# Performance work log

Hardware: AMD Instinct MI355X
Metric: run time of the kernel (lower is better)

Reference implementation:

```python
import jax, jax.numpy as jnp
import numpy as np

VOCAB = 1000
PAD_ID = 0
D = 256      # d_model
H = 256      # hidden_size
G = 4 * H    # LSTM gate width
B = 64
S = 256      # src_len
TGT = 257    # tgt_len (decode T = 256)


def setup_inputs() -> dict:
    key = jax.random.key(0)
    ks = iter(jax.random.split(key, 48))
    def p(shape, scale):
        return jax.random.normal(next(ks), shape, jnp.float32) * scale
    inp = {}
    inp['src'] = jax.random.randint(next(ks), (B, S), 1, VOCAB)    # no PAD tokens
    inp['tgt'] = jax.random.randint(next(ks), (B, TGT), 1, VOCAB)
    inp['emb'] = p((VOCAB, D), D ** -0.5).at[PAD_ID].set(0.0)       # padding_idx row zeroed
    s = 1.0 / np.sqrt(H)
    # encoder biLSTM: layer0 fwd/bwd (input D), layer1 fwd/bwd (input 2H)
    for name, din in [('e0f', D), ('e0b', D), ('e1f', 2 * H), ('e1b', 2 * H)]:
        inp[name + '_Wih'] = p((G, din), 1.0 / np.sqrt(din))
        inp[name + '_Whh'] = p((G, H), s)
        inp[name + '_bih'] = p((G,), s)
        inp[name + '_bhh'] = p((G,), s)
    # decoder LSTM: layer0 input D+2H, layer1 input H
    for name, din in [('d0', D + 2 * H), ('d1', H)]:
        inp[name + '_Wih'] = p((G, din), 1.0 / np.sqrt(din))
        inp[name + '_Whh'] = p((G, H), s)
        inp[name + '_bih'] = p((G,), s)
        inp[name + '_bhh'] = p((G,), s)
    inp['h_proj_W'] = p((H, 2 * H), 1.0 / np.sqrt(2 * H))
    inp['h_proj_b'] = p((H,), s)
    inp['c_proj_W'] = p((H, 2 * H), 1.0 / np.sqrt(2 * H))
    inp['c_proj_b'] = p((H,), s)
    inp['att_Wenc'] = p((H, 2 * H), 1.0 / np.sqrt(2 * H))
    inp['att_Wdec'] = p((H, H), s)
    inp['att_v'] = p((H,), s)
    return inp


def _cell(gates, c):
    # PyTorch gate order: i, f, g, o
    i, f, g, o = jnp.split(gates, 4, axis=-1)
    c = jax.nn.sigmoid(f) * c + jax.nn.sigmoid(i) * jnp.tanh(g)
    return jax.nn.sigmoid(o) * jnp.tanh(c), c


def _lstm(x, Wih, Whh, bih, bhh, reverse=False):
    # x: (B, S, din) -> outputs (B, S, H), final (h, c)
    Bsz = x.shape[0]
    Hd = Whh.shape[1]
    pre = jnp.swapaxes(x @ Wih.T + bih + bhh, 0, 1)  # (S, B, 4H)
    def step(carry, g):
        h, c = carry
        h, c = _cell(g + h @ Whh.T, c)
        return (h, c), h
    init = (jnp.zeros((Bsz, Hd), x.dtype), jnp.zeros((Bsz, Hd), x.dtype))
    (hT, cT), ys = jax.lax.scan(step, init, pre, reverse=reverse)
    return jnp.swapaxes(ys, 0, 1), hT, cT


def reference(src, tgt, emb,
              e0f_Wih, e0f_Whh, e0f_bih, e0f_bhh,
              e0b_Wih, e0b_Whh, e0b_bih, e0b_bhh,
              e1f_Wih, e1f_Whh, e1f_bih, e1f_bhh,
              e1b_Wih, e1b_Whh, e1b_bih, e1b_bhh,
              d0_Wih, d0_Whh, d0_bih, d0_bhh,
              d1_Wih, d1_Whh, d1_bih, d1_bhh,
              h_proj_W, h_proj_b, c_proj_W, c_proj_b,
              att_Wenc, att_Wdec, att_v):
    mask = (src == PAD_ID)                       # (B, S), all False here
    x0 = emb[src]                                # (B, S, D)
    # ---- bidirectional 2-layer encoder ----
    f0, _, _ = _lstm(x0, e0f_Wih, e0f_Whh, e0f_bih, e0f_bhh)
    b0, _, _ = _lstm(x0, e0b_Wih, e0b_Whh, e0b_bih, e0b_bhh, reverse=True)
    x1 = jnp.concatenate([f0, b0], axis=-1)      # (B, S, 2H)
    f1, hf, cf = _lstm(x1, e1f_Wih, e1f_Whh, e1f_bih, e1f_bhh)
    b1, hb, cb = _lstm(x1, e1b_Wih, e1b_Whh, e1b_bih, e1b_bhh, reverse=True)
    enc_out = jnp.concatenate([f1, b1], axis=-1)  # (B, S, 2H)
    # ---- decoder init (shared across both decoder layers) ----
    h0 = jnp.tanh(jnp.concatenate([hf, hb], -1) @ h_proj_W.T + h_proj_b)
    c0 = jnp.tanh(jnp.concatenate([cf, cb], -1) @ c_proj_W.T + c_proj_b)
    # ---- teacher-forced decode with Bahdanau attention ----
    enc_proj = enc_out @ att_Wenc.T              # (B, S, H), hoisted out of the loop
    tgt_emb = emb[tgt[:, :-1]]                   # (B, T, D)

    def dec_step(carry, xt):
        hl0, cl0, hl1, cl1 = carry
        energy = jnp.tanh(enc_proj + (hl1 @ att_Wdec.T)[:, None, :])  # (B, S, H)
        scores = energy @ att_v                                        # (B, S)
        scores = jnp.where(mask, -jnp.inf, scores)
        w = jax.nn.softmax(scores, axis=-1)
        ctx = jnp.einsum('bs,bse->be', w, enc_out)                     # (B, 2H)
        x = jnp.concatenate([xt, ctx], axis=-1)                        # (B, D+2H)
        hl0, cl0 = _cell(x @ d0_Wih.T + d0_bih + d0_bhh + hl0 @ d0_Whh.T, cl0)
        hl1, cl1 = _cell(hl0 @ d1_Wih.T + d1_bih + d1_bhh + hl1 @ d1_Whh.T, cl1)
        return (hl0, cl0, hl1, cl1), hl1

    _, outs = jax.lax.scan(dec_step, (h0, c0, h0, c0), jnp.swapaxes(tgt_emb, 0, 1))
    out = jnp.swapaxes(outs, 0, 1)               # (B, T, H); out_proj is None (H == D)
    return out @ emb.T                           # weight-tied fc_out -> (B, T, VOCAB)
```

## Files before the change

### kernel.cpp

```cpp
#include <hip/hip_runtime.h>
#include <hip/hip_bf16.h>
#include <stdint.h>

#define B_ 64
#define S_ 256
#define T_ 256
#define D_ 256
#define H_ 256
#define V_ 1000

__device__ __forceinline__ float blo(unsigned u){ return __uint_as_float(u << 16); }
__device__ __forceinline__ float bhi(unsigned u){ return __uint_as_float(u & 0xffff0000u); }
__device__ __forceinline__ float sigm(float x){ return 1.0f / (1.0f + __expf(-x)); }
__device__ __forceinline__ float tanhfast(float x){ float e = __expf(2.0f * x); return 1.0f - 2.0f / (e + 1.0f); }

__device__ __forceinline__ void cellupd(float a0, float a1, float a2, float a3, float& c, float& h){
  float cn = sigm(a1) * c + sigm(a0) * tanhfast(a2);
  c = cn;
  h = sigm(a3) * tanhfast(cn);
}

__device__ __forceinline__ float wredmax(float v){
  #pragma unroll
  for (int o = 32; o > 0; o >>= 1) v = fmaxf(v, __shfl_xor(v, o));
  return v;
}
__device__ __forceinline__ float wredsum(float v){
  #pragma unroll
  for (int o = 32; o > 0; o >>= 1) v += __shfl_xor(v, o);
  return v;
}

__device__ __forceinline__ void ast(float* p, float v){
  __hip_atomic_store(p, v, __ATOMIC_RELAXED, __HIP_MEMORY_SCOPE_AGENT);
}
__device__ __forceinline__ float ald(const float* p){
  return __hip_atomic_load(p, __ATOMIC_RELAXED, __HIP_MEMORY_SCOPE_AGENT);
}

__global__ void probe_kernel(const unsigned short* __restrict__ w, int* __restrict__ flag)
{
  int cnt = 0;
  for (int i = threadIdx.x; i < 4096; i += 64) {
    unsigned e = (w[i] >> 7) & 0xFFu;
    if (e >= 0xC0u) cnt++;
  }
  #pragma unroll
  for (int o = 32; o > 0; o >>= 1) cnt += __shfl_xor(cnt, o);
  if (threadIdx.x == 0) *flag = (cnt > 32) ? 1 : 0;
}

__device__ __forceinline__ float load_any(const void* src, int i, int isf32){
  return isf32 ? ((const float*)src)[i]
               : __uint_as_float(((unsigned)((const unsigned short*)src)[i]) << 16);
}

__global__ void conv_kernel(const void* __restrict__ src, float* __restrict__ dst, int n,
                            const int* __restrict__ flagp)
{
  int i = blockIdx.x * 256 + threadIdx.x;
  if (i >= n) return;
  dst[i] = load_any(src, i, *flagp);
}

__global__ void bias_kernel(const void* __restrict__ a, const void* __restrict__ bsrc,
                            float* __restrict__ dst, int n, const int* __restrict__ flagp)
{
  int i = blockIdx.x * 256 + threadIdx.x;
  if (i >= n) return;
  int f = *flagp;
  dst[i] = load_any(a, i, f) + load_any(bsrc, i, f);
}

__global__ void swzb_kernel(const void* __restrict__ src, unsigned short* __restrict__ dst,
                            int R, int Ks, int Kt, int c0, int perm, const int* __restrict__ flagp)
{
  int i = blockIdx.x * 256 + threadIdx.x;
  if (i >= R * Ks) return;
  int r = i / Ks;
  int k = i - r * Ks;
  int kk = k + c0;
  int Rr = r;
  if (perm) {
    int g = r >> 8, j = r & 255;
    Rr = ((j >> 4) << 6) + (g << 4) + (j & 15);
  }
  float v = load_any(src, i, *flagp);
  __hip_bfloat16 bv = __float2bfloat16(v);
  dst[(((size_t)(Rr >> 6) * (size_t)(Kt >> 3) + (size_t)(kk >> 3)) * 64 + (Rr & 63)) * 8 + (kk & 7)] =
      *(unsigned short*)&bv;
}

template<int K>
__device__ __forceinline__ float dot1w(const unsigned short* __restrict__ w, int r,
                                       const float* __restrict__ xs)
{
  constexpr int KC = K >> 3;
  const uint4* __restrict__ p = (const uint4*)w + (size_t)(r >> 6) * KC * 64 + (r & 63);
  float a = 0.0f;
  #pragma unroll 4
  for (int kc = 0; kc < KC; ++kc) {
    const uint4 q = p[(size_t)kc * 64];
    const float4 x0 = *(const float4*)(xs + kc * 8);
    const float4 x1 = *(const float4*)(xs + kc * 8 + 4);
    a += blo(q.x)*x0.x + bhi(q.x)*x0.y + blo(q.y)*x0.z + bhi(q.y)*x0.w
       + blo(q.z)*x1.x + bhi(q.z)*x1.y + blo(q.w)*x1.z + bhi(q.w)*x1.w;
  }
  return a;
}

template<int KC, int SL>
__device__ __forceinline__ void dot4s(const unsigned short* __restrict__ w, int j, int q,
                                      const float* __restrict__ xsl, float out4[4])
{
  const int lane = j & 63, wq = j >> 6;
  const uint4* __restrict__ p0 = (const uint4*)w + ((size_t)(wq     ) * KC + q * SL) * 64 + lane;
  const uint4* __restrict__ p1 = (const uint4*)w + ((size_t)(wq + 4 ) * KC + q * SL) * 64 + lane;
  const uint4* __restrict__ p2 = (const uint4*)w + ((size_t)(wq + 8 ) * KC + q * SL) * 64 + lane;
  const uint4* __restrict__ p3 = (const uint4*)w + ((size_t)(wq + 12) * KC + q * SL) * 64 + lane;
  float a0 = 0.0f, a1 = 0.0f, a2 = 0.0f, a3 = 0.0f;
  #pragma unroll 4
  for (int kc = 0; kc < SL; ++kc) {
    const float4 x0 = *(const float4*)(xsl + kc * 8);
    const float4 x1 = *(const float4*)(xsl + kc * 8 + 4);
    uint4 qq;
    qq = p0[(size_t)kc * 64];
    a0 += blo(qq.x)*x0.x + bhi(qq.x)*x0.y + blo(qq.y)*x0.z + bhi(qq.y)*x0.w
        + blo(qq.z)*x1.x + bhi(qq.z)*x1.y + blo(qq.w)*x1.z + bhi(qq.w)*x1.w;
    qq = p1[(size_t)kc * 64];
    a1 += blo(qq.x)*x0.x + bhi(qq.x)*x0.y + blo(qq.y)*x0.z + bhi(qq.y)*x0.w
        + blo(qq.z)*x1.x + bhi(qq.z)*x1.y + blo(qq.w)*x1.z + bhi(qq.w)*x1.w;
    qq = p2[(size_t)kc * 64];
    a2 += blo(qq.x)*x0.x + bhi(qq.x)*x0.y + blo(qq.y)*x0.z + bhi(qq.y)*x0.w
        + blo(qq.z)*x1.x + bhi(qq.z)*x1.y + blo(qq.w)*x1.z + bhi(qq.w)*x1.w;
    qq = p3[(size_t)kc * 64];
    a3 += blo(qq.x)*x0.x + bhi(qq.x)*x0.y + blo(qq.y)*x0.z + bhi(qq.y)*x0.w
        + blo(qq.z)*x1.x + bhi(qq.z)*x1.y + blo(qq.w)*x1.z + bhi(qq.w)*x1.w;
  }
  out4[0] = a0; out4[1] = a1; out4[2] = a2; out4[3] = a3;
}

__global__ __launch_bounds__(1024, 1) void enc0_kernel(
    const int* __restrict__ src, const float* __restrict__ emb_f,
    const unsigned short* __restrict__ wF, const unsigned short* __restrict__ wB,
    const float* __restrict__ bF, const float* __restrict__ bB,
    float* __restrict__ f0, float* __restrict__ b0)
{
  const int blk = blockIdx.x, dir = blk >> 6, b = blk & 63, tid = threadIdx.x;
  const unsigned short* w = dir ? wB : wF;
  const float* bi = dir ? bB : bF;
  float* outp = dir ? b0 : f0;
  __shared__ __align__(16) float xs[512];
  __shared__ __align__(16) float work4[4096];
  const int q = tid >> 8, j = tid & 255;
  float bias_g[4];
  if (tid < 256) {
    #pragma unroll
    for (int g = 0; g < 4; ++g) bias_g[g] = bi[g * 256 + tid];
    xs[256 + tid] = 0.0f;
  }
  float c = 0.0f, h = 0.0f;
  const size_t bS = (size_t)b * S_;
  for (int t = 0; t < S_; ++t) {
    const int tp = dir ? (S_ - 1 - t) : t;
    const int tok = src[bS + tp];
    if (tid < 256) xs[tid] = emb_f[(size_t)tok * D_ + tid];
    __syncthreads();
    float o4[4];
    dot4s<64, 16>(w, j, q, xs + q * 128, o4);
    #pragma unroll
    for (int g = 0; g < 4; ++g) work4[(g * 4 + q) * 256 + j] = o4[g];
    __syncthreads();
    if (tid < 256) {
      float gv[4];
      #pragma unroll
      for (int g = 0; g < 4; ++g)
        gv[g] = work4[(g*4+0)*256 + tid] + work4[(g*4+1)*256 + tid]
              + work4[(g*4+2)*256 + tid] + work4[(g*4+3)*256 + tid] + bias_g[g];
      cellupd(gv[0], gv[1], gv[2], gv[3], c, h);
      xs[256 + tid] = h;
      outp[(bS + tp) * H_ + tid] = h;
    }
    __syncthreads();
  }
}

__global__ __launch_bounds__(1024, 1) void enc1_kernel(
    const float* __restrict__ f0, const float* __restrict__ b0,
    const unsigned short* __restrict__ wF, const unsigned short* __restrict__ wB,
    const float* __restrict__ bF, const float* __restrict__ bB,
    float* __restrict__ enc_out, float* __restrict__ hcbuf)
{
  const int blk = blockIdx.x, dir = blk >> 6, b = blk & 63, tid = threadIdx.x;
  const unsigned short* w = dir ? wB : wF;
  const float* bi = dir ? bB : bF;
  __shared__ __align__(16) float xs[768];
  __shared__ __align__(16) float work4[4096];
  const int q = tid >> 8, j = tid & 255;
  float bias_g[4];
  if (tid < 256) {
    #pragma unroll
    for (int g = 0; g < 4; ++g) bias_g[g] = bi[g * 256 + tid];
    xs[512 + tid] = 0.0f;
  }
  float c = 0.0f, h = 0.0f;
  const size_t bS = (size_t)b * S_;
  for (int t = 0; t < S_; ++t) {
    const int tp = dir ? (S_ - 1 - t) : t;
    const size_t row = (bS + tp) * (size_t)H_;
    if (tid < 512) {
      const int jj = tid & 255;
      xs[tid] = (tid < 256) ? f0[row + jj] : b0[row + jj];
    }
    __syncthreads();
    float o4[4];
    dot4s<96, 24>(w, j, q, xs + q * 192, o4);
    #pragma unroll
    for (int g = 0; g < 4; ++g) work4[(g * 4 + q) * 256 + j] = o4[g];
    __syncthreads();
    if (tid < 256) {
      float gv[4];
      #pragma unroll
      for (int g = 0; g < 4; ++g)
        gv[g] = work4[(g*4+0)*256 + tid] + work4[(g*4+1)*256 + tid]
              + work4[(g*4+2)*256 + tid] + work4[(g*4+3)*256 + tid] + bias_g[g];
      cellupd(gv[0], gv[1], gv[2], gv[3], c, h);
      xs[512 + tid] = h;
      enc_out[(bS + tp) * 512 + dir * 256 + tid] = h;
    }
    __syncthreads();
  }
  if (tid < 256) {
    const int BH = B_ * H_;
    float* hout = hcbuf + (dir ? 2 * BH : 0);
    hout[(size_t)b * H_ + tid]      = h;
    hout[BH + (size_t)b * H_ + tid] = c;
  }
}

__global__ __launch_bounds__(256) void proj_kernel(
    const float* __restrict__ enc_out, const float* __restrict__ hcbuf,
    const unsigned short* __restrict__ wenc_s,
    const unsigned short* __restrict__ hpw_s, const unsigned short* __restrict__ cpw_s,
    const float* __restrict__ hpb_f, const float* __restrict__ cpb_f,
    float* __restrict__ epT, float* __restrict__ h0c0)
{
  __shared__ __align__(16) float xs[16 * 512];
  const int blk = blockIdx.x, tid = threadIdx.x;
  if (blk < 1024) {
    const int b = blk >> 4, s0 = (blk & 15) * 16;
    const float* srcp = enc_out + ((size_t)b * S_ + s0) * 512;
    for (int i = tid; i < 16 * 512; i += 256) xs[i] = srcp[i];
    __syncthreads();
    float acc[16];
    #pragma unroll
    for (int r = 0; r < 16; ++r) acc[r] = 0.0f;
    const uint4* p = (const uint4*)wenc_s + (size_t)(tid >> 6) * 64 * 64 + (tid & 63);
    for (int kc = 0; kc < 64; ++kc) {
      const uint4 q = p[(size_t)kc * 64];
      const float w0=blo(q.x), w1=bhi(q.x), w2=blo(q.y), w3=bhi(q.y),
                  w4=blo(q.z), w5=bhi(q.z), w6=blo(q.w), w7=bhi(q.w);
      #pragma unroll
      for (int r = 0; r < 16; ++r) {
        const float4 x0 = *(const float4*)(xs + r * 512 + kc * 8);
        const float4 x1 = *(const float4*)(xs + r * 512 + kc * 8 + 4);
        acc[r] += w0*x0.x + w1*x0.y + w2*x0.z + w3*x0.w + w4*x1.x + w5*x1.y + w6*x1.z + w7*x1.w;
      }
    }
    float* dst = epT + ((size_t)b * S_ + (size_t)tid) * 256 + s0;
    #pragma unroll
    for (int r = 0; r < 16; ++r) dst[r] = acc[r];
  } else {
    const int b = blk - 1024;
    const int BH = B_ * H_;
    xs[tid]        = hcbuf[(size_t)b * H_ + tid];
    xs[256 + tid]  = hcbuf[2 * BH + (size_t)b * H_ + tid];
    xs[512 + tid]  = hcbuf[BH + (size_t)b * H_ + tid];
    xs[768 + tid]  = hcbuf[3 * BH + (size_t)b * H_ + tid];
    __syncthreads();
    const float hv = dot1w<512>(hpw_s, tid, xs)       + hpb_f[tid];
    const float cv = dot1w<512>(cpw_s, tid, xs + 512) + cpb_f[tid];
    h0c0[(size_t)b * H_ + tid]              = tanhfast(hv);
    h0c0[(size_t)BH + (size_t)b * H_ + tid] = tanhfast(cv);
  }
}

__global__ __launch_bounds__(256) void gemb_kernel(
    const float* __restrict__ emb_f, const unsigned short* __restrict__ d0p,
    float* __restrict__ gemb)
{
  __shared__ __align__(16) float xs[16 * 256];
  const int blk = blockIdx.x, tg = blk >> 2, cg = blk & 3, tid = threadIdx.x;
  for (int i = tid; i < 16 * 256; i += 256) {
    const int tk = tg * 16 + (i >> 8);
    xs[i] = (tk < V_) ? emb_f[(size_t)tk * 256 + (i & 255)] : 0.0f;
  }
  __syncthreads();
  const int r = cg * 256 + tid;
  const uint4* p = (const uint4*)d0p + (size_t)(r >> 6) * 128 * 64 + (r & 63);
  float acc[16];
  #pragma unroll
  for (int ti = 0; ti < 16; ++ti) acc[ti] = 0.0f;
  for (int kc = 0; kc < 32; ++kc) {
    const uint4 q = p[(size_t)kc * 64];
    const float w0=blo(q.x), w1=bhi(q.x), w2=blo(q.y), w3=bhi(q.y),
                w4=blo(q.z), w5=bhi(q.z), w6=blo(q.w), w7=bhi(q.w);
    #pragma unroll
    for (int ti = 0; ti < 16; ++ti) {
      const float4 x0 = *(const float4*)(xs + ti * 256 + kc * 8);
      const float4 x1 = *(const float4*)(xs + ti * 256 + kc * 8 + 4);
      acc[ti] += w0*x0.x + w1*x0.y + w2*x0.z + w3*x0.w + w4*x1.x + w5*x1.y + w6*x1.z + w7*x1.w;
    }
  }
  #pragma unroll
  for (int ti = 0; ti < 16; ++ti) {
    const int tk = tg * 16 + ti;
    if (tk < V_) gemb[(size_t)tk * 1024 + r] = acc[ti];
  }
}

__global__ void zero_cnt_kernel(int* __restrict__ cnt)
{
  for (int i = threadIdx.x; i < 2048; i += 256) cnt[i] = 0;
}

__global__ __launch_bounds__(1024, 1) void dec_fused_kernel(
    const int* __restrict__ src, const int* __restrict__ tgt,
    const float* __restrict__ h0c0,
    const float* __restrict__ epT, const float* __restrict__ enc_out,
    const float* __restrict__ gemb,
    const unsigned short* __restrict__ wdec_s,
    const unsigned short* __restrict__ d0p, const unsigned short* __restrict__ d1p,
    const float* __restrict__ d0b, const float* __restrict__ d1b,
    const float* __restrict__ attv_f,
    float* __restrict__ dec_h,
    float* __restrict__ esc, float* __restrict__ ctxg,
    float* __restrict__ hl0g, float* __restrict__ hl1g,
    int* __restrict__ cnt)
{
  const int Bk = blockIdx.x, b = Bk >> 2, k = Bk & 3, tid = threadIdx.x;
  const int j64 = k * 64;

  __shared__ __align__(16) float epl[256 * 65];
  __shared__ __align__(16) unsigned short eol[128 * 264];
  __shared__ __align__(16) float work[1024];
  __shared__ __align__(16) float workF[1024];
  __shared__ __align__(16) float xs0[768];
  __shared__ __align__(16) float hl1s[256];
  __shared__ __align__(16) float hl0n[256];
  __shared__ __align__(16) float qloc[64];
  __shared__ __align__(16) float vv[64];
  __shared__ __align__(16) float msk[256];
  __shared__ __align__(16) float wsm[256];
  __shared__ __align__(16) float cl0s[64];
  __shared__ __align__(16) float cl1s[64];
  __shared__ float red[16];

  const float* epb = epT + (size_t)b * (S_ * 256);
  const float* eob = enc_out + (size_t)b * (S_ * 512);

  for (int i = tid; i < 256 * 64; i += 1024) {
    const int s = i & 255, jj = i >> 8;
    epl[s * 65 + jj] = epb[(size_t)(j64 + jj) * 256 + s];
  }
  for (int i = tid; i < 128 * 256; i += 1024) {
    const int dl = i & 127, s = i >> 7;
    __hip_bfloat16 bv = __float2bfloat16(eob[(size_t)s * 512 + k * 128 + dl]);
    eol[dl * 264 + s] = *(unsigned short*)&bv;
  }
  if (tid < 256) {
    msk[tid] = (src[b * 256 + tid] == 0) ? -1e30f : 0.0f;
    const float h0 = h0c0[b * 256 + tid];
    hl1s[tid] = h0;
    xs0[512 + tid] = h0;
  }
  float b0r[4], b1r[4];
  if (tid < 64) {
    vv[tid] = attv_f[j64 + tid];
    const float c0 = h0c0[B_ * H_ + b * 256 + j64 + tid];
    cl0s[tid] = c0; cl1s[tid] = c0;
    #pragma unroll
    for (int g = 0; g < 4; ++g) {
      b0r[g] = d0b[g * 256 + j64 + tid];
      b1r[g] = d1b[g * 256 + j64 + tid];
    }
  }
  __syncthreads();

  int syncno = 0;
#define ARRIVE() do {                                                                    \
    ++syncno;                                                                            \
    __syncthreads();     \
    if (tid == 0)                                                                        \
      __hip_atomic_fetch_add(&cnt[b * 32], 1, __ATOMIC_RELAXED, __HIP_MEMORY_SCOPE_AGENT); \
  } while (0)
#define WAIT() do {                                                                      \
    if (tid == 0) {                                                                      \
      while (__hip_atomic_load(&cnt[b * 32], __ATOMIC_RELAXED, __HIP_MEMORY_SCOPE_AGENT) \
             < 4 * syncno)                                                               \
        __builtin_amdgcn_s_sleep(1);                                                     \
    }                                                                                    \
    __syncthreads();                                                                     \
    asm volatile("" ::: "memory");                                                       \
  } while (0)

  const int lr = tid & 255, q4 = tid >> 8;
  const int gg4 = lr >> 6, jj4 = lr & 63;
  const uint4* __restrict__ d0pb = (const uint4*)d0p + (size_t)(gg4 * 4 + k) * 128 * 64 + jj4;
  const uint4* __restrict__ d1pb = (const uint4*)d1p + (size_t)(gg4 * 4 + k) * 64 * 64 + jj4;

  for (int t = 0; t < T_; ++t) {
    float gpre[4];
    if (tid < 64) {
      const float* ge = gemb + (size_t)tgt[b * 257 + t] * 1024;
      #pragma unroll
      for (int g = 0; g < 4; ++g)
        gpre[g] = __builtin_nontemporal_load(ge + g * 256 + j64 + tid);
    }

    {
      const int jj = tid & 63, q16 = tid >> 6;
      const uint4* p = (const uint4*)wdec_s + ((size_t)k * 32 + q16 * 2) * 64 + jj;
      const float* xsl = hl1s + q16 * 16;
      const uint4 w0 = p[0], w1 = p[64];
      const float4 xa = *(const float4*)(xsl);
      const float4 xb = *(const float4*)(xsl + 4);
      const float4 xc = *(const float4*)(xsl + 8);
      const float4 xd = *(const float4*)(xsl + 12);
      const float a =
          blo(w0.x)*xa.x + bhi(w0.x)*xa.y + blo(w0.y)*xa.z + bhi(w0.y)*xa.w
        + blo(w0.z)*xb.x + bhi(w0.z)*xb.y + blo(w0.w)*xb.z + bhi(w0.w)*xb.w
        + blo(w1.x)*xc.x + bhi(w1.x)*xc.y + blo(w1.y)*xc.z + bhi(w1.y)*xc.w
        + blo(w1.z)*xd.x + bhi(w1.z)*xd.y + blo(w1.w)*xd.z + bhi(w1.w)*xd.w;
      work[q16 * 64 + jj] = a;
    }
    __syncthreads();
    if (tid < 64) {
      float q = 0.0f;
      #pragma unroll
      for (int i = 0; i < 16; ++i) q += work[i * 64 + tid];
      qloc[tid] = q;
    }
    __syncthreads();

    {
      const int s = tid & 255, jq = tid >> 8;
      const float* ep = epl + s * 65 + jq * 16;
      const float* qv = qloc + jq * 16;
      const float* vp = vv + jq * 16;
      float a = 0.0f;
      #pragma unroll
      for (int i = 0; i < 16; ++i)
        a += vp[i] * tanhfast(ep[i] + qv[i]);
      work[jq * 256 + s] = a;
    }
    __syncthreads();
    if (tid < 256)
      ast(&esc[b * 1024 + k * 256 + tid],
          work[tid] + work[256 + tid] + work[512 + tid] + work[768 + tid]);
    ARRIVE();

    {
      const uint4* p = d0pb + (size_t)(96 + q4 * 8) * 64;
      const float* xsl = xs0 + 512 + q4 * 64;
      float a = 0.0f;
      #pragma unroll
      for (int kc = 0; kc < 8; ++kc) {
        const uint4 w = p[(size_t)kc * 64];
        const float4 x0 = *(const float4*)(xsl + kc * 8);
        const float4 x1 = *(const float4*)(xsl + kc * 8 + 4);
        a += blo(w.x)*x0.x + bhi(w.x)*x0.y + blo(w.y)*x0.z + bhi(w.y)*x0.w
           + blo(w.z)*x1.x + bhi(w.z)*x1.y + blo(w.w)*x1.z + bhi(w.w)*x1.w;
      }
      work[q4 * 256 + lr] = a;
    }
    WAIT();

    {
      float e = -1e30f;
      if (tid < 256) {
        const float* eb = esc + b * 1024;
        e = ald(&eb[tid]) + ald(&eb[256 + tid]) + ald(&eb[512 + tid]) + ald(&eb[768 + tid])
          + msk[tid];
      }
      const float m0 = wredmax(e);
      if (tid < 256 && (tid & 63) == 0) red[tid >> 6] = m0;
      __syncthreads();
      const float m = fmaxf(fmaxf(red[0], red[1]), fmaxf(red[2], red[3]));
      const float pe = (tid < 256) ? __expf(e - m) : 0.0f;
      const float ss = wredsum(pe);
      if (tid < 256 && (tid & 63) == 0) red[4 + (tid >> 6)] = ss;
      __syncthreads();
      const float inv = 1.0f / ((red[4] + red[5]) + (red[6] + red[7]));
      if (tid < 256) wsm[tid] = pe * inv;
    }
    __syncthreads();

    {
      const int dq = tid & 127, sg = tid >> 7;
      const uint4* er = (const uint4*)(eol + dq * 264 + sg * 32);
      const float* wp = wsm + sg * 32;
      float a = 0.0f;
      #pragma unroll
      for (int i4 = 0; i4 < 4; ++i4) {
        const uint4 q = er[i4];
        const float* w8 = wp + i4 * 8;
        a += blo(q.x)*w8[0] + bhi(q.x)*w8[1] + blo(q.y)*w8[2] + bhi(q.y)*w8[3]
           + blo(q.z)*w8[4] + bhi(q.z)*w8[5] + blo(q.w)*w8[6] + bhi(q.w)*w8[7];
      }
      workF[sg * 128 + dq] = a;
    }
    __syncthreads();
    if (tid < 128) {
      float a = 0.0f;
      #pragma unroll
      for (int g = 0; g < 8; ++g) a += workF[g * 128 + tid];
      ast(&ctxg[b * 512 + k * 128 + tid], a);
    }
    ARRIVE();

    {
      const uint4* p = d1pb + (size_t)(32 + q4 * 8) * 64;
      const float* xsl = hl1s + q4 * 64;
      float a = 0.0f;
      #pragma unroll
      for (int kc = 0; kc < 8; ++kc) {
        const uint4 w = p[(size_t)kc * 64];
        const float4 x0 = *(const float4*)(xsl + kc * 8);
        const float4 x1 = *(const float4*)(xsl + kc * 8 + 4);
        a += blo(w.x)*x0.x + bhi(w.x)*x0.y + blo(w.y)*x0.z + bhi(w.y)*x0.w
           + blo(w.z)*x1.x + bhi(w.z)*x1.y + blo(w.w)*x1.z + bhi(w.w)*x1.w;
      }
      workF[q4 * 256 + lr] = a;
    }
    WAIT();
    if (tid < 512) xs0[tid] = ald(&ctxg[b * 512 + tid]);
    __syncthreads();

    {
      const uint4* p = d0pb + (size_t)(32 + q4 * 16) * 64;
      const float* xsl = xs0 + q4 * 128;
      float a = 0.0f;
      #pragma unroll 8
      for (int kc = 0; kc < 16; ++kc) {
        const uint4 w = p[(size_t)kc * 64];
        const float4 x0 = *(const float4*)(xsl + kc * 8);
        const float4 x1 = *(const float4*)(xsl + kc * 8 + 4);
        a += blo(w.x)*x0.x + bhi(w.x)*x0.y + blo(w.y)*x0.z + bhi(w.y)*x0.w
           + blo(w.z)*x1.x + bhi(w.z)*x1.y + blo(w.w)*x1.z + bhi(w.w)*x1.w;
      }
      work[q4 * 256 + lr] += a;
    }
    __syncthreads();
    if (tid < 64) {
      float gv[4];
      #pragma unroll
      for (int g = 0; g < 4; ++g) {
        const int r = g * 64 + tid;
        gv[g] = work[r] + work[256 + r] + work[512 + r] + work[768 + r]
              + b0r[g] + gpre[g];
      }
      float c = cl0s[tid], h;
      cellupd(gv[0], gv[1], gv[2], gv[3], c, h);
      cl0s[tid] = c;
      ast(&hl0g[b * 256 + j64 + tid], h);
    }
    ARRIVE();
    WAIT();
    if (tid < 256) {
      const float hv = ald(&hl0g[b * 256 + tid]);
      hl0n[tid] = hv;
      xs0[512 + tid] = hv;
    }
    __syncthreads();

    {
      const uint4* p = d1pb + (size_t)(q4 * 8) * 64;
      const float* xsl = hl0n + q4 * 64;
      float a = 0.0f;
      #pragma unroll
      for (int kc = 0; kc < 8; ++kc) {
        const uint4 w = p[(size_t)kc * 64];
        const float4 x0 = *(const float4*)(xsl + kc * 8);
        const float4 x1 = *(const float4*)(xsl + kc * 8 + 4);
        a += blo(w.x)*x0.x + bhi(w.x)*x0.y + blo(w.y)*x0.z + bhi(w.y)*x0.w
           + blo(w.z)*x1.x + bhi(w.z)*x1.y + blo(w.w)*x1.z + bhi(w.w)*x1.w;
      }
      workF[q4 * 256 + lr] += a;
    }
    __syncthreads();
    if (tid < 64) {
      float gv[4];
      #pragma unroll
      for (int g = 0; g < 4; ++g) {
        const int r = g * 64 + tid;
        gv[g] = workF[r] + workF[256 + r] + workF[512 + r] + workF[768 + r] + b1r[g];
      }
      float c = cl1s[tid], h;
      cellupd(gv[0], gv[1], gv[2], gv[3], c, h);
      cl1s[tid] = c;
      ast(&hl1g[b * 256 + j64 + tid], h);
      __builtin_nontemporal_store(h, &dec_h[((size_t)b * T_ + t) * H_ + j64 + tid]);
    }
    ARRIVE();
    WAIT();
    if (tid < 256) hl1s[tid] = ald(&hl1g[b * 256 + tid]);
    __syncthreads();
  }
#undef ARRIVE
#undef WAIT
}

__global__ __launch_bounds__(256) void out_kernel(
    const float* __restrict__ dec_h, const unsigned short* __restrict__ emb_s,
    void* __restrict__ out, const int* __restrict__ flagp)
{
  __shared__ __align__(16) float hs[16 * 256];
  const int blk = blockIdx.x, tid = threadIdx.x;
  const int isf32 = *flagp;
  const float* srcp = dec_h + (size_t)blk * (16 * 256);
  for (int i = tid; i < 16 * 256; i += 256) hs[i] = srcp[i];
  __syncthreads();
  #pragma unroll
  for (int vi = 0; vi < 4; ++vi) {
    const int v = tid + vi * 256;
    if (v < V_) {
      const uint4* p = (const uint4*)emb_s + (size_t)(v >> 6) * 32 * 64 + (v & 63);
      float acc[16];
      #pragma unroll
      for (int r = 0; r < 16; ++r) acc[r] = 0.0f;
      for (int kc = 0; kc < 32; ++kc) {
        const uint4 q = p[(size_t)kc * 64];
        const float w0=blo(q.x), w1=bhi(q.x), w2=blo(q.y), w3=bhi(q.y),
                    w4=blo(q.z), w5=bhi(q.z), w6=blo(q.w), w7=bhi(q.w);
        #pragma unroll
        for (int r = 0; r < 16; ++r) {
          const float4 x0 = *(const float4*)(hs + r * 256 + kc * 8);
          const float4 x1 = *(const float4*)(hs + r * 256 + kc * 8 + 4);
          acc[r] += w0*x0.x + w1*x0.y + w2*x0.z + w3*x0.w + w4*x1.x + w5*x1.y + w6*x1.z + w7*x1.w;
        }
      }
      const size_t rowbase = (size_t)blk * 16;
      if (isf32) {
        float* o = (float*)out;
        #pragma unroll
        for (int r = 0; r < 16; ++r) o[(rowbase + r) * V_ + v] = acc[r];
      } else {
        __hip_bfloat16* o = (__hip_bfloat16*)out;
        #pragma unroll
        for (int r = 0; r < 16; ++r) o[(rowbase + r) * V_ + v] = __float2bfloat16(acc[r]);
      }
    }
  }
}

extern "C" void kernel_launch(void* const* d_in, const int* in_sizes, int n_in,
                              void* d_out, int out_size, void* d_ws, size_t ws_size,
                              hipStream_t stream)
{
  (void)in_sizes; (void)n_in; (void)out_size; (void)ws_size;
  const int* src = (const int*)d_in[0];
  const int* tgt = (const int*)d_in[1];

  char* base = (char*)d_ws;
  int* flag = (int*)base;
  float* ws = (float*)(base + 256);
  size_t off = 0;
  float* f0      = ws + off; off += (size_t)B_ * S_ * H_;
  float* b0      = ws + off; off += (size_t)B_ * S_ * H_;
  float* enc_out = ws + off; off += (size_t)B_ * S_ * 2 * H_;
  float* hcbuf   = ws + off; off += 4 * (size_t)B_ * H_;
  float* h0c0    = ws + off; off += 2 * (size_t)B_ * H_;
  float* emb_f   = ws + off; off += (size_t)V_ * D_;
  float* gemb    = ws + off; off += (size_t)V_ * 1024;
  float* esc     = ws + off; off += (size_t)B_ * S_ * 4;
  float* ctxg    = ws + off; off += (size_t)B_ * 512;
  float* hl0g    = ws + off; off += (size_t)B_ * H_;
  float* hl1g    = ws + off; off += (size_t)B_ * H_;
  int*   cntp    = (int*)(ws + off); off += 2048;
  float* e0f_b   = ws + off; off += 1024;
  float* e0b_b   = ws + off; off += 1024;
  float* e1f_b   = ws + off; off += 1024;
  float* e1b_b   = ws + off; off += 1024;
  float* d0_b    = ws + off; off += 1024;
  float* d1_b    = ws + off; off += 1024;
  float* hpb_f   = ws + off; off += 256;
  float* cpb_f   = ws + off; off += 256;
  float* attv_f  = ws + off; off += 256;
  unsigned short* us = (unsigned short*)(ws + off);
  size_t uo = 0;
  unsigned short* e0f_s  = us + uo; uo += (size_t)1024 * 512;
  unsigned short* e0b_s  = us + uo; uo += (size_t)1024 * 512;
  unsigned short* e1f_s  = us + uo; uo += (size_t)1024 * 768;
  unsigned short* e1b_s  = us + uo; uo += (size_t)1024 * 768;
  unsigned short* d0p_s  = us + uo; uo += (size_t)1024 * 1024;
  unsigned short* d1p_s  = us + uo; uo += (size_t)1024 * 512;
  unsigned short* wdec_s = us + uo; uo += (size_t)256 * 256;
  unsigned short* wenc_s = us + uo; uo += (size_t)256 * 512;
  unsigned short* hpw_s  = us + uo; uo += (size_t)256 * 512;
  unsigned short* cpw_s  = us + uo; uo += (size_t)256 * 512;
  unsigned short* emb_s  = us + uo; uo += (size_t)1024 * 256;
  float* dec_h = f0;
  float* epT   = b0;

  hipLaunchKernelGGL(probe_kernel, dim3(1), dim3(64), 0, stream,
                     (const unsigned short*)d_in[3], flag);

  auto swz = [&](int idx, unsigned short* dst, int R, int Ks, int Kt, int c0, int perm){
    const int n = R * Ks;
    hipLaunchKernelGGL(swzb_kernel, dim3((n + 255) / 256), dim3(256), 0, stream,
                       d_in[idx], dst, R, Ks, Kt, c0, perm, flag);
  };
  auto bias2 = [&](int ia, int ib, float* dst, int n){
    hipLaunchKernelGGL(bias_kernel, dim3((n + 255) / 256), dim3(256), 0, stream,
                       d_in[ia], d_in[ib], dst, n, flag);
  };

  hipLaunchKernelGGL(conv_kernel, dim3((V_ * D_ + 255) / 256), dim3(256), 0, stream,
                     d_in[2], emb_f, V_ * D_, flag);
  hipLaunchKernelGGL(conv_kernel, dim3(1), dim3(256), 0, stream, d_in[28], hpb_f, 256, flag);
  hipLaunchKernelGGL(conv_kernel, dim3(1), dim3(256), 0, stream, d_in[30], cpb_f, 256, flag);
  hipLaunchKernelGGL(conv_kernel, dim3(1), dim3(256), 0, stream, d_in[33], attv_f, 256, flag);
  bias2(5, 6, e0f_b, 1024);   bias2(9, 10, e0b_b, 1024);
  bias2(13, 14, e1f_b, 1024); bias2(17, 18, e1b_b, 1024);
  bias2(21, 22, d0_b, 1024);  bias2(25, 26, d1_b, 1024);
  swz(3,  e0f_s, 1024, 256, 512, 0, 0);   swz(4,  e0f_s, 1024, 256, 512, 256, 0);
  swz(7,  e0b_s, 1024, 256, 512, 0, 0);   swz(8,  e0b_s, 1024, 256, 512, 256, 0);
  swz(11, e1f_s, 1024, 512, 768, 0, 0);   swz(12, e1f_s, 1024, 256, 768, 512, 0);
  swz(15, e1b_s, 1024, 512, 768, 0, 0);   swz(16, e1b_s, 1024, 256, 768, 512, 0);
  swz(19, d0p_s, 1024, 768, 1024, 0, 0);  swz(20, d0p_s, 1024, 256, 1024, 768, 0);
  swz(23, d1p_s, 1024, 256, 512, 0, 0);   swz(24, d1p_s, 1024, 256, 512, 256, 0);
  swz(32, wdec_s, 256, 256, 256, 0, 0);
  swz(31, wenc_s, 256, 512, 512, 0, 0);
  swz(27, hpw_s, 256, 512, 512, 0, 0);
  swz(29, cpw_s, 256, 512, 512, 0, 0);
  swz(2,  emb_s, 1000, 256, 256, 0, 0);

  hipLaunchKernelGGL(gemb_kernel, dim3(252), dim3(256), 0, stream, emb_f, d0p_s, gemb);

  hipLaunchKernelGGL(enc0_kernel, dim3(128), dim3(1024), 0, stream,
                     src, emb_f, e0f_s, e0b_s, e0f_b, e0b_b, f0, b0);
  hipLaunchKernelGGL(enc1_kernel, dim3(128), dim3(1024), 0, stream,
                     f0, b0, e1f_s, e1b_s, e1f_b, e1b_b, enc_out, hcbuf);
  hipLaunchKernelGGL(proj_kernel, dim3(1088), dim3(256), 0, stream,
                     enc_out, hcbuf, wenc_s, hpw_s, cpw_s, hpb_f, cpb_f, epT, h0c0);

  hipLaunchKernelGGL(zero_cnt_kernel, dim3(1), dim3(256), 0, stream, cntp);

  {
    const int* srcp_ = src; const int* tgtp_ = tgt;
    const float* h0c0_ = h0c0; const float* epT_ = epT; const float* eo_ = enc_out;
    const float* gemb_ = gemb;
    const unsigned short* wdec_ = wdec_s;
    const unsigned short* d0p_ = d0p_s; const unsigned short* d1p_ = d1p_s;
    const float* d0b_ = d0_b; const float* d1b_ = d1_b; const float* attv_ = attv_f;
    float* dech_ = dec_h; float* esc_ = esc; float* ctxg_ = ctxg;
    float* hl0g_ = hl0g; float* hl1g_ = hl1g; int* cnt_ = cntp;
    void* kargs[] = {
      (void*)&srcp_, (void*)&tgtp_, (void*)&h0c0_, (void*)&epT_, (void*)&eo_,
      (void*)&gemb_, (void*)&wdec_, (void*)&d0p_, (void*)&d1p_,
      (void*)&d0b_, (void*)&d1b_, (void*)&attv_,
      (void*)&dech_, (void*)&esc_, (void*)&ctxg_, (void*)&hl0g_, (void*)&hl1g_, (void*)&cnt_
    };
    hipError_t e = hipLaunchCooperativeKernel((const void*)dec_fused_kernel,
                                              dim3(256), dim3(1024), kargs, 0, stream);
    if (e != hipSuccess) {
      hipLaunchKernelGGL(dec_fused_kernel, dim3(256), dim3(1024), 0, stream,
                         srcp_, tgtp_, h0c0_, epT_, eo_, gemb_, wdec_, d0p_, d1p_,
                         d0b_, d1b_, attv_, dech_, esc_, ctxg_, hl0g_, hl1g_, cnt_);
    }
  }

  hipLaunchKernelGGL(out_kernel, dim3(1024), dim3(256), 0, stream,
                     dec_h, emb_s, d_out, flag);
}
```

Baseline: 13.75 ms.

## Split decoder per batch across 8 smaller blocks with XCD-aware mapping

```diff
diff --git a/kernel.cpp b/kernel.cpp
--- a/kernel.cpp
+++ b/kernel.cpp
@@ -324,7 +324,7 @@
   for (int i = threadIdx.x; i < 2048; i += 256) cnt[i] = 0;
 }
 
-__global__ __launch_bounds__(1024, 1) void dec_fused_kernel(
+__global__ __launch_bounds__(512, 4) void dec_fused_kernel(
     const int* __restrict__ src, const int* __restrict__ tgt,
     const float* __restrict__ h0c0,
     const float* __restrict__ epT, const float* __restrict__ enc_out,
@@ -338,34 +338,36 @@
     float* __restrict__ hl0g, float* __restrict__ hl1g,
     int* __restrict__ cnt)
 {
-  const int Bk = blockIdx.x, b = Bk >> 2, k = Bk & 3, tid = threadIdx.x;
-  const int j64 = k * 64;
-
-  __shared__ __align__(16) float epl[256 * 65];
-  __shared__ __align__(16) unsigned short eol[128 * 264];
-  __shared__ __align__(16) float work[1024];
-  __shared__ __align__(16) float workF[1024];
+  const int Bk = blockIdx.x, tid = threadIdx.x;
+  const int xcd = Bk >> 6, i64 = Bk & 63;
+  const int b = xcd * 8 + (i64 & 7), k = i64 >> 3;
+  const int j32 = k * 32, d64 = k * 64;
+
+  __shared__ __align__(16) float epl[256 * 33];
+  __shared__ __align__(16) unsigned short eol[64 * 264];
+  __shared__ __align__(16) float work[512];
+  __shared__ __align__(16) float workF[512];
   __shared__ __align__(16) float xs0[768];
   __shared__ __align__(16) float hl1s[256];
   __shared__ __align__(16) float hl0n[256];
-  __shared__ __align__(16) float qloc[64];
-  __shared__ __align__(16) float vv[64];
+  __shared__ __align__(16) float qloc[32];
+  __shared__ __align__(16) float vv[32];
   __shared__ __align__(16) float msk[256];
   __shared__ __align__(16) float wsm[256];
-  __shared__ __align__(16) float cl0s[64];
-  __shared__ __align__(16) float cl1s[64];
+  __shared__ __align__(16) float cl0s[32];
+  __shared__ __align__(16) float cl1s[32];
   __shared__ float red[16];
 
   const float* epb = epT + (size_t)b * (S_ * 256);
   const float* eob = enc_out + (size_t)b * (S_ * 512);
 
-  for (int i = tid; i < 256 * 64; i += 1024) {
+  for (int i = tid; i < 256 * 32; i += 512) {
     const int s = i & 255, jj = i >> 8;
-    epl[s * 65 + jj] = epb[(size_t)(j64 + jj) * 256 + s];
-  }
-  for (int i = tid; i < 128 * 256; i += 1024) {
-    const int dl = i & 127, s = i >> 7;
-    __hip_bfloat16 bv = __float2bfloat16(eob[(size_t)s * 512 + k * 128 + dl]);
+    epl[s * 33 + jj] = epb[(size_t)(j32 + jj) * 256 + s];
+  }
+  for (int i = tid; i < 64 * 256; i += 512) {
+    const int dl = i & 63, s = i >> 6;
+    __hip_bfloat16 bv = __float2bfloat16(eob[(size_t)s * 512 + d64 + dl]);
     eol[dl * 264 + s] = *(unsigned short*)&bv;
   }
   if (tid < 256) {
@@ -375,14 +377,14 @@
     xs0[512 + tid] = h0;
   }
   float b0r[4], b1r[4];
-  if (tid < 64) {
-    vv[tid] = attv_f[j64 + tid];
-    const float c0 = h0c0[B_ * H_ + b * 256 + j64 + tid];
+  if (tid < 32) {
+    vv[tid] = attv_f[j32 + tid];
+    const float c0 = h0c0[B_ * H_ + b * 256 + j32 + tid];
     cl0s[tid] = c0; cl1s[tid] = c0;
     #pragma unroll
     for (int g = 0; g < 4; ++g) {
-      b0r[g] = d0b[g * 256 + j64 + tid];
-      b1r[g] = d1b[g * 256 + j64 + tid];
+      b0r[g] = d0b[g * 256 + j32 + tid];
+      b1r[g] = d1b[g * 256 + j32 + tid];
     }
   }
   __syncthreads();
@@ -397,32 +399,35 @@
 #define WAIT() do {                                                                      \
     if (tid == 0) {                                                                      \
       while (__hip_atomic_load(&cnt[b * 32], __ATOMIC_RELAXED, __HIP_MEMORY_SCOPE_AGENT) \
-             < 4 * syncno)                                                               \
+             < 8 * syncno)                                                               \
         __builtin_amdgcn_s_sleep(1);                                                     \
     }                                                                                    \
     __syncthreads();                                                                     \
     asm volatile("" ::: "memory");                                                       \
   } while (0)
 
-  const int lr = tid & 255, q4 = tid >> 8;
-  const int gg4 = lr >> 6, jj4 = lr & 63;
-  const uint4* __restrict__ d0pb = (const uint4*)d0p + (size_t)(gg4 * 4 + k) * 128 * 64 + jj4;
-  const uint4* __restrict__ d1pb = (const uint4*)d1p + (size_t)(gg4 * 4 + k) * 64 * 64 + jj4;
+  const int lr = tid & 127, q4 = tid >> 7;
+  const int g4 = lr >> 5, jj32 = lr & 31;
+  const int lane = ((k & 1) << 5) + jj32;
+  const int rg0 = g4 * 4 + (k >> 1);
+  const uint4* __restrict__ d0pb = (const uint4*)d0p + (size_t)rg0 * 128 * 64 + lane;
+  const uint4* __restrict__ d1pb = (const uint4*)d1p + (size_t)rg0 * 64 * 64 + lane;
+  const int jjA = tid & 31, q16 = tid >> 5;
+  const uint4* __restrict__ wAp = (const uint4*)wdec_s
+      + ((size_t)(k >> 1) * 32 + q16 * 2) * 64 + (((k & 1) << 5) + jjA);
 
   for (int t = 0; t < T_; ++t) {
     float gpre[4];
-    if (tid < 64) {
+    if (tid < 32) {
       const float* ge = gemb + (size_t)tgt[b * 257 + t] * 1024;
       #pragma unroll
       for (int g = 0; g < 4; ++g)
-        gpre[g] = __builtin_nontemporal_load(ge + g * 256 + j64 + tid);
+        gpre[g] = __builtin_nontemporal_load(ge + g * 256 + j32 + tid);
     }
 
     {
-      const int jj = tid & 63, q16 = tid >> 6;
-      const uint4* p = (const uint4*)wdec_s + ((size_t)k * 32 + q16 * 2) * 64 + jj;
       const float* xsl = hl1s + q16 * 16;
-      const uint4 w0 = p[0], w1 = p[64];
+      const uint4 w0 = wAp[0], w1 = wAp[64];
       const float4 xa = *(const float4*)(xsl);
       const float4 xb = *(const float4*)(xsl + 4);
       const float4 xc = *(const float4*)(xsl + 8);
@@ -432,20 +437,20 @@
         + blo(w0.z)*xb.x + bhi(w0.z)*xb.y + blo(w0.w)*xb.z + bhi(w0.w)*xb.w
         + blo(w1.x)*xc.x + bhi(w1.x)*xc.y + blo(w1.y)*xc.z + bhi(w1.y)*xc.w
         + blo(w1.z)*xd.x + bhi(w1.z)*xd.y + blo(w1.w)*xd.z + bhi(w1.w)*xd.w;
-      work[q16 * 64 + jj] = a;
-    }
-    __syncthreads();
-    if (tid < 64) {
+      work[q16 * 32 + jjA] = a;
+    }
+    __syncthreads();
+    if (tid < 32) {
       float q = 0.0f;
       #pragma unroll
-      for (int i = 0; i < 16; ++i) q += work[i * 64 + tid];
+      for (int i = 0; i < 16; ++i) q += work[i * 32 + tid];
       qloc[tid] = q;
     }
     __syncthreads();
 
     {
       const int s = tid & 255, jq = tid >> 8;
-      const float* ep = epl + s * 65 + jq * 16;
+      const float* ep = epl + s * 33 + jq * 16;
       const float* qv = qloc + jq * 16;
       const float* vp = vv + jq * 16;
       float a = 0.0f;
@@ -456,8 +461,7 @@
     }
     __syncthreads();
     if (tid < 256)
-      ast(&esc[b * 1024 + k * 256 + tid],
-          work[tid] + work[256 + tid] + work[512 + tid] + work[768 + tid]);
+      ast(&esc[b * 2048 + k * 256 + tid], work[tid] + work[256 + tid]);
     ARRIVE();
 
     {
@@ -472,16 +476,17 @@
         a += blo(w.x)*x0.x + bhi(w.x)*x0.y + blo(w.y)*x0.z + bhi(w.y)*x0.w
            + blo(w.z)*x1.x + bhi(w.z)*x1.y + blo(w.w)*x1.z + bhi(w.w)*x1.w;
       }
-      work[q4 * 256 + lr] = a;
+      work[q4 * 128 + lr] = a;
     }
     WAIT();
 
     {
       float e = -1e30f;
       if (tid < 256) {
-        const float* eb = esc + b * 1024;
-        e = ald(&eb[tid]) + ald(&eb[256 + tid]) + ald(&eb[512 + tid]) + ald(&eb[768 + tid])
-          + msk[tid];
+        const float* eb = esc + b * 2048;
+        e = msk[tid];
+        #pragma unroll
+        for (int kk = 0; kk < 8; ++kk) e += ald(&eb[kk * 256 + tid]);
       }
       const float m0 = wredmax(e);
       if (tid < 256 && (tid & 63) == 0) red[tid >> 6] = m0;
@@ -497,7 +502,7 @@
     __syncthreads();
 
     {
-      const int dq = tid & 127, sg = tid >> 7;
+      const int dq = tid & 63, sg = tid >> 6;
       const uint4* er = (const uint4*)(eol + dq * 264 + sg * 32);
       const float* wp = wsm + sg * 32;
       float a = 0.0f;
@@ -508,14 +513,14 @@
         a += blo(q.x)*w8[0] + bhi(q.x)*w8[1] + blo(q.y)*w8[2] + bhi(q.y)*w8[3]
            + blo(q.z)*w8[4] + bhi(q.z)*w8[5] + blo(q.w)*w8[6] + bhi(q.w)*w8[7];
       }
-      workF[sg * 128 + dq] = a;
-    }
-    __syncthreads();
-    if (tid < 128) {
+      workF[sg * 64 + dq] = a;
+    }
+    __syncthreads();
+    if (tid < 64) {
       float a = 0.0f;
       #pragma unroll
-      for (int g = 0; g < 8; ++g) a += workF[g * 128 + tid];
-      ast(&ctxg[b * 512 + k * 128 + tid], a);
+      for (int g = 0; g < 8; ++g) a += workF[g * 64 + tid];
+      ast(&ctxg[b * 512 + d64 + tid], a);
     }
     ARRIVE();
 
@@ -531,10 +536,10 @@
         a += blo(w.x)*x0.x + bhi(w.x)*x0.y + blo(w.y)*x0.z + bhi(w.y)*x0.w
            + blo(w.z)*x1.x + bhi(w.z)*x1.y + blo(w.w)*x1.z + bhi(w.w)*x1.w;
       }
-      workF[q4 * 256 + lr] = a;
+      workF[q4 * 128 + lr] = a;
     }
     WAIT();
-    if (tid < 512) xs0[tid] = ald(&ctxg[b * 512 + tid]);
+    xs0[tid] = ald(&ctxg[b * 512 + tid]);
     __syncthreads();
 
     {
@@ -549,21 +554,21 @@
         a += blo(w.x)*x0.x + bhi(w.x)*x0.y + blo(w.y)*x0.z + bhi(w.y)*x0.w
            + blo(w.z)*x1.x + bhi(w.z)*x1.y + blo(w.w)*x1.z + bhi(w.w)*x1.w;
       }
-      work[q4 * 256 + lr] += a;
-    }
-    __syncthreads();
-    if (tid < 64) {
+      work[q4 * 128 + lr] += a;
+    }
+    __syncthreads();
+    if (tid < 32) {
       float gv[4];
       #pragma unroll
       for (int g = 0; g < 4; ++g) {
-        const int r = g * 64 + tid;
-        gv[g] = work[r] + work[256 + r] + work[512 + r] + work[768 + r]
+        const int r = g * 32 + tid;
+        gv[g] = work[r] + work[128 + r] + work[256 + r] + work[384 + r]
               + b0r[g] + gpre[g];
       }
       float c = cl0s[tid], h;
       cellupd(gv[0], gv[1], gv[2], gv[3], c, h);
       cl0s[tid] = c;
-      ast(&hl0g[b * 256 + j64 + tid], h);
+      ast(&hl0g[b * 256 + j32 + tid], h);
     }
     ARRIVE();
     WAIT();
@@ -586,21 +591,21 @@
         a += blo(w.x)*x0.x + bhi(w.x)*x0.y + blo(w.y)*x0.z + bhi(w.y)*x0.w
            + blo(w.z)*x1.x + bhi(w.z)*x1.y + blo(w.w)*x1.z + bhi(w.w)*x1.w;
       }
-      workF[q4 * 256 + lr] += a;
-    }
-    __syncthreads();
-    if (tid < 64) {
+      workF[q4 * 128 + lr] += a;
+    }
+    __syncthreads();
+    if (tid < 32) {
       float gv[4];
       #pragma unroll
       for (int g = 0; g < 4; ++g) {
-        const int r = g * 64 + tid;
-        gv[g] = workF[r] + workF[256 + r] + workF[512 + r] + workF[768 + r] + b1r[g];
+        const int r = g * 32 + tid;
+        gv[g] = workF[r] + workF[128 + r] + workF[256 + r] + workF[384 + r] + b1r[g];
       }
       float c = cl1s[tid], h;
       cellupd(gv[0], gv[1], gv[2], gv[3], c, h);
       cl1s[tid] = c;
-      ast(&hl1g[b * 256 + j64 + tid], h);
-      __builtin_nontemporal_store(h, &dec_h[((size_t)b * T_ + t) * H_ + j64 + tid]);
+      ast(&hl1g[b * 256 + j32 + tid], h);
+      __builtin_nontemporal_store(h, &dec_h[((size_t)b * T_ + t) * H_ + j32 + tid]);
     }
     ARRIVE();
     WAIT();
@@ -673,7 +678,7 @@
   float* h0c0    = ws + off; off += 2 * (size_t)B_ * H_;
   float* emb_f   = ws + off; off += (size_t)V_ * D_;
   float* gemb    = ws + off; off += (size_t)V_ * 1024;
-  float* esc     = ws + off; off += (size_t)B_ * S_ * 4;
+  float* esc     = ws + off; off += (size_t)B_ * S_ * 8;
   float* ctxg    = ws + off; off += (size_t)B_ * 512;
   float* hl0g    = ws + off; off += (size_t)B_ * H_;
   float* hl1g    = ws + off; off += (size_t)B_ * H_;
@@ -763,9 +768,9 @@
       (void*)&dech_, (void*)&esc_, (void*)&ctxg_, (void*)&hl0g_, (void*)&hl1g_, (void*)&cnt_
     };
     hipError_t e = hipLaunchCooperativeKernel((const void*)dec_fused_kernel,
-                                              dim3(256), dim3(1024), kargs, 0, stream);
+                                              dim3(512), dim3(512), kargs, 0, stream);
     if (e != hipSuccess) {
-      hipLaunchKernelGGL(dec_fused_kernel, dim3(256), dim3(1024), 0, stream,
+      hipLaunchKernelGGL(dec_fused_kernel, dim3(512), dim3(512), 0, stream,
                          srcp_, tgtp_, h0c0_, epT_, eo_, gemb_, wdec_, d0p_, d1p_,
                          d0b_, d1b_, attv_, dech_, esc_, ctxg_, hl0g_, hl1g_, cnt_);
     }
```

After: 14.83 ms. 1.08x slower.
